# Performance work log

Hardware: AMD Instinct MI355X
Metric: run time of the kernel (lower is better)

## Reference

```python
import jax, jax.numpy as jnp
import numpy as np

B, L, D, H = 4, 4096, 1024, 16
DH = D // H  # 64


def setup_inputs() -> dict:
    key = jax.random.key(0)
    k1, k2, k3, k4 = jax.random.split(key, 4)
    x = jax.random.normal(k1, (B, L, D), dtype=jnp.float32)
    # torch.nn.Linear weights stored as [out_features, in_features]
    Wq = jax.random.normal(k2, (D, D), dtype=jnp.float32) * 0.02
    Wkv = jax.random.normal(k3, (2 * D, D), dtype=jnp.float32) * 0.02
    Wout = jax.random.normal(k4, (D, D), dtype=jnp.float32) * 0.02
    return {"x": x, "Wq": Wq, "Wkv": Wkv, "Wout": Wout}


def reference(x, Wq, Wkv, Wout):
    b, l, d = x.shape
    # q: (B, L, H, Dh) -- NOTE: source never transposes to (B,H,L,Dh)
    q = (x @ Wq.T).reshape(b, l, H, DH)
    kv = (x @ Wkv.T).reshape(b, l, H, 2, DH)
    k = kv[..., 0, :]  # (B, L, H, Dh)
    v = kv[..., 1, :]  # (B, L, H, Dh)
    # Faithful to source: matmul over the last two dims -> (B, L, H, H)
    # i.e. attention over the HEAD axis at each (b, l) position.
    attn = jnp.einsum('blhd,bljd->blhj', q, k) / jnp.sqrt(jnp.float32(DH))
    attn = jax.nn.softmax(attn, axis=-1)
    out = jnp.einsum('blhj,bljd->blhd', attn, v).reshape(b, l, d)
    return out @ Wout.T
```

## Files before the change

kernel.cpp:

```cpp
#include <hip/hip_runtime.h>

typedef unsigned short ushort_t;
typedef __attribute__((ext_vector_type(8))) __bf16 bf16x8;
typedef __attribute__((ext_vector_type(4))) float f32x4;

#define NB 4
#define NL 4096
#define ND 1024
#define NH 16
#define NDH 64
#define NM (NB*NL)

__device__ __forceinline__ ushort_t f2bf(float f) {
  unsigned u = __builtin_bit_cast(unsigned, f);
  u += 0x7fffu + ((u >> 16) & 1u);
  return (ushort_t)(u >> 16);
}

__device__ __forceinline__ void gl_lds16(const void* g, void* l) {
  __builtin_amdgcn_global_load_lds(
      (const __attribute__((address_space(1))) unsigned*)g,
      (__attribute__((address_space(3))) unsigned*)l, 16, 0, 0);
}

__global__ __launch_bounds__(256) void k_cvt4(
    const float* __restrict__ x, const float* __restrict__ Wq,
    const float* __restrict__ Wkv, const float* __restrict__ Wout,
    ushort_t* __restrict__ xb, ushort_t* __restrict__ Wcat,
    ushort_t* __restrict__ Woutb)
{
  int i = blockIdx.x * 256 + threadIdx.x;
  const int stride = gridDim.x * 256;
  for (; i < 5242880; i += stride) {
    const float4* src; ushort4* dst; int off;
    if (i < 4194304)      { src = (const float4*)x;    dst = (ushort4*)xb;                 off = i; }
    else if (i < 4456448) { src = (const float4*)Wq;   dst = (ushort4*)Wcat;               off = i - 4194304; }
    else if (i < 4980736) { src = (const float4*)Wkv;  dst = (ushort4*)(Wcat + 1048576);   off = i - 4456448; }
    else                  { src = (const float4*)Wout; dst = (ushort4*)Woutb;              off = i - 4980736; }
    float4 v = src[off];
    ushort4 o;
    o.x = f2bf(v.x); o.y = f2bf(v.y); o.z = f2bf(v.z); o.w = f2bf(v.w);
    dst[off] = o;
  }
}

template<int MODE>
__global__ __launch_bounds__(512, 2) void k_gemm256(
    const ushort_t* __restrict__ A, const ushort_t* __restrict__ Bt,
    void* __restrict__ Cout, int N, int gridN)
{
  __shared__ __align__(16) ushort_t As[2][16384];
  __shared__ __align__(16) ushort_t Bs[2][16384];
  constexpr int K = 1024;
  const int tid = threadIdx.x;
  const int lane = tid & 63, wv = tid >> 6;
  const int wm = wv >> 2, wn = wv & 3;
  const int l15 = lane & 15, lhi = lane >> 4;

  const int nb = gridDim.x * gridDim.y;
  const int lid = blockIdx.y * gridDim.x + blockIdx.x;
  const int perx = nb >> 3;
  const int xcd = lid & 7, l = lid >> 3;
  const int stC = gridN >> 2;
  const int st = l >> 4, wi = l & 15;
  const int rp = xcd * (perx / gridN) + (st / stC) * 4 + (wi >> 2);
  const int cp = (st % stC) * 4 + (wi & 3);
  const int rowBase = rp * 256;
  const int colBase = cp * 256;

  const ushort_t* Abase = A + (size_t)rowBase * K;
  const ushort_t* Bbase = Bt + (size_t)colBase * K;

  const int so = tid >> 3;
  const int scol = (tid & 7) * 8;
  const int ssw = (so & 7) << 3;
  const int offG = so * K + (scol ^ ssw);
  const int sbase = wv * 512;

#define STAGE(dst, KT) do { \
  const ushort_t* Ag = Abase + (KT)*64 + offG; \
  const ushort_t* Bg = Bbase + (KT)*64 + offG; \
  gl_lds16(Ag,          &As[dst][sbase]); \
  gl_lds16(Ag + 65536,  &As[dst][4096  + sbase]); \
  gl_lds16(Ag + 131072, &As[dst][8192  + sbase]); \
  gl_lds16(Ag + 196608, &As[dst][12288 + sbase]); \
  gl_lds16(Bg,          &Bs[dst][sbase]); \
  gl_lds16(Bg + 65536,  &Bs[dst][4096  + sbase]); \
  gl_lds16(Bg + 131072, &Bs[dst][8192  + sbase]); \
  gl_lds16(Bg + 196608, &Bs[dst][12288 + sbase]); \
} while(0)

  const int fsw = (l15 & 7) << 3;
  const int kc0 = (lhi * 8) ^ fsw;
  const int kc1 = (32 + lhi * 8) ^ fsw;

  f32x4 acc[8][4] = {};

#define HALF(CUR, KC) do { \
  bf16x8 af[8], bfr[4]; \
  _Pragma("unroll") for (int i_ = 0; i_ < 8; ++i_) \
    af[i_] = *(const bf16x8*)&As[CUR][(wm*128 + i_*16 + l15)*64 + (KC)]; \
  _Pragma("unroll") for (int j_ = 0; j_ < 4; ++j_) \
    bfr[j_] = *(const bf16x8*)&Bs[CUR][(wn*64 + j_*16 + l15)*64 + (KC)]; \
  __builtin_amdgcn_sched_barrier(0); \
  __builtin_amdgcn_s_setprio(1); \
  _Pragma("unroll") for (int i_ = 0; i_ < 8; ++i_) \
  _Pragma("unroll") for (int j_ = 0; j_ < 4; ++j_) \
    acc[i_][j_] = __builtin_amdgcn_mfma_f32_16x16x32_bf16(af[i_], bfr[j_], acc[i_][j_], 0, 0, 0); \
  __builtin_amdgcn_s_setprio(0); \
} while(0)

  STAGE(0, 0);
  asm volatile("s_waitcnt vmcnt(0)" ::: "memory");
  __builtin_amdgcn_s_barrier();

  for (int t = 0; t < 16; ++t) {
    const int cur = t & 1;
    if (t < 15) STAGE(cur ^ 1, t + 1);
    HALF(cur, kc0);
    HALF(cur, kc1);
    if (t < 15) {
      asm volatile("s_waitcnt vmcnt(0)" ::: "memory");
      __builtin_amdgcn_s_barrier();
    }
  }
#undef HALF
#undef STAGE

  const int orow = rowBase + wm * 128 + lhi * 4;
  const int ocol = colBase + wn * 64 + l15;
#pragma unroll
  for (int i = 0; i < 8; ++i)
#pragma unroll
    for (int j = 0; j < 4; ++j)
#pragma unroll
      for (int rr = 0; rr < 4; ++rr) {
        int gr = orow + i * 16 + rr;
        int gc = ocol + j * 16;
        if (MODE == 2) ((float*)Cout)[(size_t)gr * N + gc] = acc[i][j][rr];
        else           ((ushort_t*)Cout)[(size_t)gr * N + gc] = f2bf(acc[i][j][rr]);
      }
}

__global__ __launch_bounds__(256) void k_attn(
    const ushort_t* __restrict__ qkv, ushort_t* __restrict__ aout)
{
  __shared__ __align__(16) ushort_t qs[4][16*72];
  __shared__ __align__(16) ushort_t kvs[4][16*136];
  __shared__ __align__(16) ushort_t ps[4][16*40];
  __shared__ __align__(16) ushort_t os[4][1024];
  const int tid = threadIdx.x, lane = tid & 63, wave = tid >> 6;
  const int t = blockIdx.x * 4 + wave;
  const int l15 = lane & 15, lhi = lane >> 4;
  const ushort_t* row = qkv + (size_t)t * 3072;

#pragma unroll
  for (int c = 0; c < 6; ++c) {
    int c8 = c * 64 + lane;
    bf16x8 v = *(const bf16x8*)(row + c8 * 8);
    if (c8 < 128) {
      int h = c8 >> 3, off = (c8 & 7) * 8;
      *(bf16x8*)&qs[wave][h*72 + off] = v;
    } else {
      int e = c8 * 8 - 1024;
      int h = e >> 7, off = e & 127;
      *(bf16x8*)&kvs[wave][h*136 + off] = v;
    }
  }
  if (lane < 16) {
    bf16x8 z = {};
    *(bf16x8*)&ps[wave][lane*40 + 16] = z;
    *(bf16x8*)&ps[wave][lane*40 + 24] = z;
  }
  __syncthreads();

  bf16x8 aq0 = *(const bf16x8*)&qs[wave][l15*72 + lhi*8];
  bf16x8 aq1 = *(const bf16x8*)&qs[wave][l15*72 + 32 + lhi*8];
  bf16x8 bk0 = *(const bf16x8*)&kvs[wave][l15*136 + lhi*8];
  bf16x8 bk1 = *(const bf16x8*)&kvs[wave][l15*136 + 32 + lhi*8];
  f32x4 s = {};
  s = __builtin_amdgcn_mfma_f32_16x16x32_bf16(aq0, bk0, s, 0, 0, 0);
  s = __builtin_amdgcn_mfma_f32_16x16x32_bf16(aq1, bk1, s, 0, 0, 0);

#pragma unroll
  for (int r = 0; r < 4; ++r) {
    float sv = s[r] * 0.125f;
    float tm = sv;
#pragma unroll
    for (int off = 1; off < 16; off <<= 1) tm = fmaxf(tm, __shfl_xor(tm, off, 64));
    float p = __expf(sv - tm);
    float rs = p;
#pragma unroll
    for (int off = 1; off < 16; off <<= 1) rs += __shfl_xor(rs, off, 64);
    p /= rs;
    ps[wave][(lhi*4 + r)*40 + l15] = f2bf(p);
  }
  __syncthreads();

  bf16x8 pa = *(const bf16x8*)&ps[wave][l15*40 + lhi*8];
#pragma unroll
  for (int dt = 0; dt < 4; ++dt) {
    bf16x8 vb;
#pragma unroll
    for (int i = 0; i < 8; ++i) {
      int j = (lhi*8 + i) & 15;
      vb[i] = __builtin_bit_cast(__bf16, kvs[wave][j*136 + 64 + dt*16 + l15]);
    }
    f32x4 o = {};
    o = __builtin_amdgcn_mfma_f32_16x16x32_bf16(pa, vb, o, 0, 0, 0);
#pragma unroll
    for (int r = 0; r < 4; ++r)
      os[wave][(lhi*4 + r)*64 + dt*16 + l15] = f2bf(o[r]);
  }
  __syncthreads();

  ushort_t* orow = aout + (size_t)t * 1024;
#pragma unroll
  for (int c = 0; c < 2; ++c) {
    int idx = (c*64 + lane) * 8;
    *(bf16x8*)(orow + idx) = *(const bf16x8*)&os[wave][idx];
  }
}

extern "C" void kernel_launch(void* const* d_in, const int* in_sizes, int n_in,
                              void* d_out, int out_size, void* d_ws, size_t ws_size,
                              hipStream_t stream) {
  const float* x    = (const float*)d_in[0];
  const float* Wq   = (const float*)d_in[1];
  const float* Wkv  = (const float*)d_in[2];
  const float* Wout = (const float*)d_in[3];
  float* out = (float*)d_out;

  ushort_t* ws    = (ushort_t*)d_ws;
  ushort_t* xb    = ws;
  ushort_t* Wcat  = xb + 16777216;
  ushort_t* Woutb = Wcat + 3145728;
  ushort_t* qkv   = Woutb + 1048576;
  ushort_t* aout  = xb;

  k_cvt4<<<2048, 256, 0, stream>>>(x, Wq, Wkv, Wout, xb, Wcat, Woutb);

  dim3 g1(12, 64);
  k_gemm256<0><<<g1, 512, 0, stream>>>(xb, Wcat, qkv, 3072, 12);

  k_attn<<<NM/4, 256, 0, stream>>>(qkv, aout);

  dim3 g3(4, 64);
  k_gemm256<2><<<g3, 512, 0, stream>>>(aout, Woutb, out, 1024, 4);
}
```

Before: 192.8 us.

## Fuse fp32-to-bf16 conversion of x into the QKV GEMM A-tile loads

The QKV projection GEMM now reads x directly in fp32, converts to bf16 in registers, and writes the swizzled tile into LDS, while B still streams via direct global-to-LDS loads. The standalone conversion kernel now only converts weights, which removes a full pass that wrote and re-read a bf16 copy of x. In exchange, the GEMM fetches twice the bytes for A per tile and uses more registers, with the conversion work interleaved between the two MFMA halves.

```diff
diff --git a/kernel.cpp b/kernel.cpp
--- a/kernel.cpp
+++ b/kernel.cpp
@@ -23,20 +23,18 @@
       (__attribute__((address_space(3))) unsigned*)l, 16, 0, 0);
 }
 
-__global__ __launch_bounds__(256) void k_cvt4(
-    const float* __restrict__ x, const float* __restrict__ Wq,
-    const float* __restrict__ Wkv, const float* __restrict__ Wout,
-    ushort_t* __restrict__ xb, ushort_t* __restrict__ Wcat,
-    ushort_t* __restrict__ Woutb)
+__global__ __launch_bounds__(256) void k_cvtW(
+    const float* __restrict__ Wq, const float* __restrict__ Wkv,
+    const float* __restrict__ Wout,
+    ushort_t* __restrict__ Wcat, ushort_t* __restrict__ Woutb)
 {
   int i = blockIdx.x * 256 + threadIdx.x;
   const int stride = gridDim.x * 256;
-  for (; i < 5242880; i += stride) {
+  for (; i < 1048576; i += stride) {
     const float4* src; ushort4* dst; int off;
-    if (i < 4194304)      { src = (const float4*)x;    dst = (ushort4*)xb;                 off = i; }
-    else if (i < 4456448) { src = (const float4*)Wq;   dst = (ushort4*)Wcat;               off = i - 4194304; }
-    else if (i < 4980736) { src = (const float4*)Wkv;  dst = (ushort4*)(Wcat + 1048576);   off = i - 4456448; }
-    else                  { src = (const float4*)Wout; dst = (ushort4*)Woutb;              off = i - 4980736; }
+    if (i < 262144)      { src = (const float4*)Wq;   dst = (ushort4*)Wcat;               off = i; }
+    else if (i < 786432) { src = (const float4*)Wkv;  dst = (ushort4*)(Wcat + 1048576);   off = i - 262144; }
+    else                 { src = (const float4*)Wout; dst = (ushort4*)Woutb;              off = i - 786432; }
     float4 v = src[off];
     ushort4 o;
     o.x = f2bf(v.x); o.y = f2bf(v.y); o.z = f2bf(v.z); o.w = f2bf(v.w);
@@ -44,9 +42,9 @@
   }
 }
 
-template<int MODE>
+template<int MODE, int AFP32>
 __global__ __launch_bounds__(512, 2) void k_gemm256(
-    const ushort_t* __restrict__ A, const ushort_t* __restrict__ Bt,
+    const void* __restrict__ Avoid, const ushort_t* __restrict__ Bt,
     void* __restrict__ Cout, int N, int gridN)
 {
   __shared__ __align__(16) ushort_t As[2][16384];
@@ -68,7 +66,6 @@
   const int rowBase = rp * 256;
   const int colBase = cp * 256;
 
-  const ushort_t* Abase = A + (size_t)rowBase * K;
   const ushort_t* Bbase = Bt + (size_t)colBase * K;
 
   const int so = tid >> 3;
@@ -77,7 +74,13 @@
   const int offG = so * K + (scol ^ ssw);
   const int sbase = wv * 512;
 
-#define STAGE(dst, KT) do { \
+  const int ar0 = tid >> 3;
+  const int ac0 = (tid & 7) * 8;
+  const int awsw = ac0 ^ ((ar0 & 7) << 3);
+  const float* Af = (AFP32 ? (const float*)Avoid : nullptr);
+  const ushort_t* Abase = (AFP32 ? nullptr : (const ushort_t*)Avoid + (size_t)rowBase * K);
+
+#define STAGE_AB(dst, KT) do { \
   const ushort_t* Ag = Abase + (KT)*64 + offG; \
   const ushort_t* Bg = Bbase + (KT)*64 + offG; \
   gl_lds16(Ag,          &As[dst][sbase]); \
@@ -88,6 +91,32 @@
   gl_lds16(Bg + 65536,  &Bs[dst][4096  + sbase]); \
   gl_lds16(Bg + 131072, &Bs[dst][8192  + sbase]); \
   gl_lds16(Bg + 196608, &Bs[dst][12288 + sbase]); \
+} while(0)
+
+#define STAGE_B(dst, KT) do { \
+  const ushort_t* Bg = Bbase + (KT)*64 + offG; \
+  gl_lds16(Bg,          &Bs[dst][sbase]); \
+  gl_lds16(Bg + 65536,  &Bs[dst][4096  + sbase]); \
+  gl_lds16(Bg + 131072, &Bs[dst][8192  + sbase]); \
+  gl_lds16(Bg + 196608, &Bs[dst][12288 + sbase]); \
+} while(0)
+
+  float4 a4[8];
+#define ALOAD(KT) do { \
+  _Pragma("unroll") for (int c_ = 0; c_ < 4; ++c_) { \
+    const float* p_ = Af + (size_t)(rowBase + c_*64 + ar0) * 1024 + (KT)*64 + ac0; \
+    a4[c_*2]   = *(const float4*)p_; \
+    a4[c_*2+1] = *(const float4*)(p_ + 4); } \
+  asm volatile("" ::: "memory");   \
+} while(0)
+
+#define AWRITE(dst) do { \
+  _Pragma("unroll") for (int c_ = 0; c_ < 4; ++c_) { \
+    bf16x8 w_; \
+    _Pragma("unroll") for (int e_ = 0; e_ < 4; ++e_) { \
+      w_[e_]   = __builtin_bit_cast(__bf16, f2bf(a4[c_*2][e_])); \
+      w_[e_+4] = __builtin_bit_cast(__bf16, f2bf(a4[c_*2+1][e_])); } \
+    *(bf16x8*)&As[dst][(c_*64 + ar0)*64 + awsw] = w_; } \
 } while(0)
 
   const int fsw = (l15 & 7) << 3;
@@ -110,22 +139,48 @@
   __builtin_amdgcn_s_setprio(0); \
 } while(0)
 
-  STAGE(0, 0);
-  asm volatile("s_waitcnt vmcnt(0)" ::: "memory");
+  if constexpr (AFP32) {
+    ALOAD(0);
+    STAGE_B(0, 0);
+    asm volatile("s_waitcnt vmcnt(4)" ::: "memory");
+    AWRITE(0);
+    asm volatile("s_waitcnt vmcnt(0) lgkmcnt(0)" ::: "memory");
+  } else {
+    STAGE_AB(0, 0);
+    asm volatile("s_waitcnt vmcnt(0)" ::: "memory");
+  }
   __builtin_amdgcn_s_barrier();
 
   for (int t = 0; t < 16; ++t) {
     const int cur = t & 1;
-    if (t < 15) STAGE(cur ^ 1, t + 1);
-    HALF(cur, kc0);
-    HALF(cur, kc1);
-    if (t < 15) {
-      asm volatile("s_waitcnt vmcnt(0)" ::: "memory");
-      __builtin_amdgcn_s_barrier();
+    const int nxt = cur ^ 1;
+    if constexpr (AFP32) {
+      if (t < 15) { ALOAD(t + 1); STAGE_B(nxt, t + 1); }
+      HALF(cur, kc0);
+      if (t < 15) {
+        asm volatile("s_waitcnt vmcnt(4)" ::: "memory");
+        AWRITE(nxt);
+      }
+      HALF(cur, kc1);
+      if (t < 15) {
+        asm volatile("s_waitcnt vmcnt(0) lgkmcnt(0)" ::: "memory");
+        __builtin_amdgcn_s_barrier();
+      }
+    } else {
+      if (t < 15) STAGE_AB(nxt, t + 1);
+      HALF(cur, kc0);
+      HALF(cur, kc1);
+      if (t < 15) {
+        asm volatile("s_waitcnt vmcnt(0)" ::: "memory");
+        __builtin_amdgcn_s_barrier();
+      }
     }
   }
 #undef HALF
-#undef STAGE
+#undef ALOAD
+#undef AWRITE
+#undef STAGE_AB
+#undef STAGE_B
 
   const int orow = rowBase + wm * 128 + lhi * 4;
   const int ocol = colBase + wn * 64 + l15;
@@ -232,19 +287,18 @@
   float* out = (float*)d_out;
 
   ushort_t* ws    = (ushort_t*)d_ws;
-  ushort_t* xb    = ws;
-  ushort_t* Wcat  = xb + 16777216;
+  ushort_t* aout  = ws;
+  ushort_t* Wcat  = aout + 16777216;
   ushort_t* Woutb = Wcat + 3145728;
   ushort_t* qkv   = Woutb + 1048576;
-  ushort_t* aout  = xb;
-
-  k_cvt4<<<2048, 256, 0, stream>>>(x, Wq, Wkv, Wout, xb, Wcat, Woutb);
+
+  k_cvtW<<<512, 256, 0, stream>>>(Wq, Wkv, Wout, Wcat, Woutb);
 
   dim3 g1(12, 64);
-  k_gemm256<0><<<g1, 512, 0, stream>>>(xb, Wcat, qkv, 3072, 12);
+  k_gemm256<0, 1><<<g1, 512, 0, stream>>>(x, Wcat, qkv, 3072, 12);
 
   k_attn<<<NM/4, 256, 0, stream>>>(qkv, aout);
 
   dim3 g3(4, 64);
-  k_gemm256<2><<<g3, 512, 0, stream>>>(aout, Woutb, out, 1024, 4);
-}
+  k_gemm256<2, 0><<<g3, 512, 0, stream>>>(aout, Woutb, out, 1024, 4);
+}
```

New measurement: 209.3 us. +8.6%, slower.
